# Kernel optimization log

Hardware: AMD Instinct MI355X
Metric: run time of the kernel (lower is better)

Reference implementation:

```python
import jax, jax.numpy as jnp
import numpy as np

N = 150000
K = 64
C = 128


def setup_inputs() -> dict:
    key = jax.random.key(0)
    k1, k2, k3, k4 = jax.random.split(key, 4)
    H = 512
    W = 512
    pX = jax.random.randint(k1, (N,), 0, W, dtype=jnp.int32)
    pY = jax.random.randint(k2, (N,), 0, H, dtype=jnp.int32)
    vertMask = jax.random.normal(k3, (K, N), dtype=jnp.float32)
    feature = jax.random.normal(k4, (C, K), dtype=jnp.float32)
    return {"H": H, "W": W, "pX": pX, "pY": pY, "vertMask": vertMask, "feature": feature}


def reference(H, W, pX, pY, vertMask, feature):
    # [C, K] @ [K, N] -> [C, N]
    vals = jnp.matmul(feature, vertMask)
    out = jnp.zeros((feature.shape[0], H, W), dtype=feature.dtype)
    # scatter per-vertex features into the dense HxW canvas at irregular coords
    return out.at[:, pY, pX].set(vals)
```

## Files before the change

### kernel.cpp

```cpp
#include <hip/hip_runtime.h>

constexpr int KK = 64;
constexpr int CC = 128;

typedef float f32x4 __attribute__((ext_vector_type(4)));
typedef short short8 __attribute__((ext_vector_type(8)));
typedef unsigned short ushort_t;
typedef ushort_t ushort8 __attribute__((ext_vector_type(8)));

__device__ inline ushort_t f2bf(float f) {
    union { float f; unsigned u; } v; v.f = f;
    unsigned r = v.u + 0x7FFFu + ((v.u >> 16) & 1u);
    return (ushort_t)(r >> 16);
}

__global__ __launch_bounds__(256) void transpose_bf16(
        const float* __restrict__ vm, ushort_t* __restrict__ vmT, int N) {
    __shared__ float tile[KK][KK + 1];
    int t = threadIdx.x;
    int n0 = blockIdx.x * KK;
    int lane = t & 63;
    int wv = t >> 6;
    int n = n0 + lane;
    #pragma unroll
    for (int r = 0; r < 16; ++r) {
        int k = r * 4 + wv;
        tile[k][lane] = (n < N) ? vm[(size_t)k * N + n] : 0.f;
    }
    __syncthreads();
    #pragma unroll
    for (int r = 0; r < 16; ++r) {
        int nl = r * 4 + wv;
        int nn = n0 + nl;
        if (nn < N) vmT[(size_t)nn * KK + lane] = f2bf(tile[lane][nl]);
    }
}

__global__ __launch_bounds__(256) void scatter_winner(
        const int* __restrict__ pX, const int* __restrict__ pY,
        const int* __restrict__ pW, int* __restrict__ winner, int N) {
    int i = blockIdx.x * 256 + threadIdx.x;
    if (i < N) atomicMax(&winner[pY[i] * pW[0] + pX[i]], i);
}

__global__ __launch_bounds__(256, 4) void produce_mfma(
        const int* __restrict__ winner, const ushort_t* __restrict__ vmT,
        const float* __restrict__ feature, float* __restrict__ out, int HW) {
    __shared__ ushort_t ldsB[256][72];
    int t = threadIdx.x;
    int p0 = blockIdx.x * 256;
    int wv = t >> 6;
    int L = t & 63;
    int lm = L & 15, q = L >> 4;
    int m0 = wv * 32;

    short8 afrag[2][2];
    #pragma unroll
    for (int mt = 0; mt < 2; ++mt)
        #pragma unroll
        for (int kh = 0; kh < 2; ++kh) {
            const float* fp = feature + (size_t)(m0 + mt * 16 + lm) * KK + kh * 32 + q * 8;
            f32x4 x0 = *(const f32x4*)fp;
            f32x4 x1 = *(const f32x4*)(fp + 4);
            short8 s;
            s[0] = (short)f2bf(x0[0]); s[1] = (short)f2bf(x0[1]);
            s[2] = (short)f2bf(x0[2]); s[3] = (short)f2bf(x0[3]);
            s[4] = (short)f2bf(x1[0]); s[5] = (short)f2bf(x1[1]);
            s[6] = (short)f2bf(x1[2]); s[7] = (short)f2bf(x1[3]);
            afrag[mt][kh] = s;
        }

    int w = (p0 + t < HW) ? winner[p0 + t] : -1;
    if (w >= 0) {
        const ushort8* src = (const ushort8*)(vmT + (size_t)w * KK);
        #pragma unroll
        for (int i = 0; i < 8; ++i) *(ushort8*)&ldsB[t][i * 8] = src[i];
    } else {
        ushort8 z = {0, 0, 0, 0, 0, 0, 0, 0};
        #pragma unroll
        for (int i = 0; i < 8; ++i) *(ushort8*)&ldsB[t][i * 8] = z;
    }
    __syncthreads();

    #pragma unroll 4
    for (int nt = 0; nt < 16; ++nt) {
        short8 b0 = *(const short8*)&ldsB[nt * 16 + lm][q * 8];
        short8 b1 = *(const short8*)&ldsB[nt * 16 + lm][32 + q * 8];
        f32x4 acc0 = {0.f, 0.f, 0.f, 0.f};
        f32x4 acc1 = {0.f, 0.f, 0.f, 0.f};
        acc0 = __builtin_amdgcn_mfma_f32_16x16x32_bf16(afrag[0][0], b0, acc0, 0, 0, 0);
        acc0 = __builtin_amdgcn_mfma_f32_16x16x32_bf16(afrag[0][1], b1, acc0, 0, 0, 0);
        acc1 = __builtin_amdgcn_mfma_f32_16x16x32_bf16(afrag[1][0], b0, acc1, 0, 0, 0);
        acc1 = __builtin_amdgcn_mfma_f32_16x16x32_bf16(afrag[1][1], b1, acc1, 0, 0, 0);
        int pc = p0 + nt * 16 + lm;
        #pragma unroll
        for (int r = 0; r < 4; ++r) {
            out[(size_t)(m0 + q * 4 + r) * HW + pc] = acc0[r];
            out[(size_t)(m0 + 16 + q * 4 + r) * HW + pc] = acc1[r];
        }
    }
}

extern "C" void kernel_launch(void* const* d_in, const int* in_sizes, int n_in,
                              void* d_out, int out_size, void* d_ws, size_t ws_size,
                              hipStream_t stream) {
    const int* dW = (const int*)d_in[1];
    const int* pX = (const int*)d_in[2];
    const int* pY = (const int*)d_in[3];
    const float* vm = (const float*)d_in[4];
    const float* feat = (const float*)d_in[5];
    float* out = (float*)d_out;

    int N = in_sizes[2];
    int HW = out_size / CC;

    int* winner = (int*)d_ws;
    size_t winBytes = (((size_t)HW * sizeof(int)) + 255) & ~(size_t)255;
    ushort_t* vmT = (ushort_t*)((char*)d_ws + winBytes);

    hipMemsetAsync(winner, 0xFF, (size_t)HW * sizeof(int), stream);
    hipLaunchKernelGGL(transpose_bf16, dim3((N + KK - 1) / KK), dim3(256), 0, stream,
                       vm, vmT, N);
    hipLaunchKernelGGL(scatter_winner, dim3((N + 255) / 256), dim3(256), 0, stream,
                       pX, pY, dW, winner, N);
    hipLaunchKernelGGL(produce_mfma, dim3(HW / 256), dim3(256), 0, stream,
                       winner, vmT, feat, out, HW);
}
```

Baseline: 197.3 us.

## Fuse transpose and winner scatter into one launch; read B rows directly

Merges the bf16 transpose and the atomicMax winner scatter into one kernel whose grid is split into tile blocks and scatter blocks, removing a launch and letting the two phases overlap. The produce kernel drops its LDS staging and barrier and instead loads each MFMA B fragment straight from the gathered vmT row in global memory. Empty pixels point at a padded zero row at index N, which the transpose now writes because its bounds check was removed (the last tile fills the pad with zeros). This relies on the workspace being large enough for the padded row, and the direct gather issues more scattered global loads than the single coalesced LDS staging did.

```diff
diff --git a/kernel.cpp b/kernel.cpp
--- a/kernel.cpp
+++ b/kernel.cpp
@@ -6,7 +6,6 @@
 typedef float f32x4 __attribute__((ext_vector_type(4)));
 typedef short short8 __attribute__((ext_vector_type(8)));
 typedef unsigned short ushort_t;
-typedef ushort_t ushort8 __attribute__((ext_vector_type(8)));
 
 __device__ inline ushort_t f2bf(float f) {
     union { float f; unsigned u; } v; v.f = f;
@@ -14,11 +13,20 @@
     return (ushort_t)(r >> 16);
 }
 
-__global__ __launch_bounds__(256) void transpose_bf16(
-        const float* __restrict__ vm, ushort_t* __restrict__ vmT, int N) {
+__global__ __launch_bounds__(256) void prep_fused(
+        const float* __restrict__ vm, ushort_t* __restrict__ vmT,
+        const int* __restrict__ pX, const int* __restrict__ pY,
+        const int* __restrict__ pW, int* __restrict__ winner,
+        int N, int nTile) {
+    int b = blockIdx.x;
+    int t = threadIdx.x;
+    if (b >= nTile) {
+        int i = (b - nTile) * 256 + t;
+        if (i < N) atomicMax(&winner[pY[i] * pW[0] + pX[i]], i);
+        return;
+    }
     __shared__ float tile[KK][KK + 1];
-    int t = threadIdx.x;
-    int n0 = blockIdx.x * KK;
+    int n0 = b * KK;
     int lane = t & 63;
     int wv = t >> 6;
     int n = n0 + lane;
@@ -31,22 +39,14 @@
     #pragma unroll
     for (int r = 0; r < 16; ++r) {
         int nl = r * 4 + wv;
-        int nn = n0 + nl;
-        if (nn < N) vmT[(size_t)nn * KK + lane] = f2bf(tile[lane][nl]);
+        vmT[(size_t)(n0 + nl) * KK + lane] = f2bf(tile[lane][nl]);
     }
-}
-
-__global__ __launch_bounds__(256) void scatter_winner(
-        const int* __restrict__ pX, const int* __restrict__ pY,
-        const int* __restrict__ pW, int* __restrict__ winner, int N) {
-    int i = blockIdx.x * 256 + threadIdx.x;
-    if (i < N) atomicMax(&winner[pY[i] * pW[0] + pX[i]], i);
 }
 
 __global__ __launch_bounds__(256, 4) void produce_mfma(
         const int* __restrict__ winner, const ushort_t* __restrict__ vmT,
-        const float* __restrict__ feature, float* __restrict__ out, int HW) {
-    __shared__ ushort_t ldsB[256][72];
+        const float* __restrict__ feature, float* __restrict__ out,
+        int HW, int zrow) {
     int t = threadIdx.x;
     int p0 = blockIdx.x * 256;
     int wv = t >> 6;
@@ -70,22 +70,18 @@
             afrag[mt][kh] = s;
         }
 
-    int w = (p0 + t < HW) ? winner[p0 + t] : -1;
-    if (w >= 0) {
-        const ushort8* src = (const ushort8*)(vmT + (size_t)w * KK);
-        #pragma unroll
-        for (int i = 0; i < 8; ++i) *(ushort8*)&ldsB[t][i * 8] = src[i];
-    } else {
-        ushort8 z = {0, 0, 0, 0, 0, 0, 0, 0};
-        #pragma unroll
-        for (int i = 0; i < 8; ++i) *(ushort8*)&ldsB[t][i * 8] = z;
+    int wc[16];
+    #pragma unroll
+    for (int nt = 0; nt < 16; ++nt) {
+        int w = winner[p0 + nt * 16 + lm];
+        wc[nt] = (w >= 0) ? w : zrow;
     }
-    __syncthreads();
 
     #pragma unroll 4
     for (int nt = 0; nt < 16; ++nt) {
-        short8 b0 = *(const short8*)&ldsB[nt * 16 + lm][q * 8];
-        short8 b1 = *(const short8*)&ldsB[nt * 16 + lm][32 + q * 8];
+        const short8* row = (const short8*)(vmT + (size_t)wc[nt] * KK);
+        short8 b0 = row[q];
+        short8 b1 = row[4 + q];
         f32x4 acc0 = {0.f, 0.f, 0.f, 0.f};
         f32x4 acc1 = {0.f, 0.f, 0.f, 0.f};
         acc0 = __builtin_amdgcn_mfma_f32_16x16x32_bf16(afrag[0][0], b0, acc0, 0, 0, 0);
@@ -118,11 +114,12 @@
     size_t winBytes = (((size_t)HW * sizeof(int)) + 255) & ~(size_t)255;
     ushort_t* vmT = (ushort_t*)((char*)d_ws + winBytes);
 
+    int nTile = (N + KK - 1) / KK;
+    int nScat = (N + 255) / 256;
+
     hipMemsetAsync(winner, 0xFF, (size_t)HW * sizeof(int), stream);
-    hipLaunchKernelGGL(transpose_bf16, dim3((N + KK - 1) / KK), dim3(256), 0, stream,
-                       vm, vmT, N);
-    hipLaunchKernelGGL(scatter_winner, dim3((N + 255) / 256), dim3(256), 0, stream,
-                       pX, pY, dW, winner, N);
+    hipLaunchKernelGGL(prep_fused, dim3(nTile + nScat), dim3(256), 0, stream,
+                       vm, vmT, pX, pY, dW, winner, N, nTile);
     hipLaunchKernelGGL(produce_mfma, dim3(HW / 256), dim3(256), 0, stream,
-                       winner, vmT, feat, out, HW);
+                       winner, vmT, feat, out, HW, N);
 }
```

New measurement: 200.0 us. About the same (+1.4%).
